# Kernel optimization log

Measured on AMD Instinct MI355X. Metric: run time of the kernel, lower is better.

## Reference

```python
import jax, jax.numpy as jnp
import numpy as np
import math

NUM_HEAD = 8
QK_DIM = 32       # in_dim // num_head
V_DIM = 32
KV_STRIDE = 2
Q_STRIDE = 1
LOCAL_RANGE = 16  # hard_range
POS_DIM = 256     # position_embedding_dim (= in_dim)
POS_MAG = 1.0
WAVE = 1000.0


def _position_feats(h, w, h_kv, w_kv, fcx_w, fcy_w):
    # sinusoidal embedding of (query_pos - key_pos), then linear projection per head
    fr = jnp.arange(POS_DIM // 4, dtype=jnp.float32)
    dim_mat = WAVE ** (4.0 / POS_DIM * fr)                 # (POS_DIM/4,)

    def emb(n_q, n_kv):
        diff = (jnp.arange(n_q, dtype=jnp.float32)[:, None] * Q_STRIDE
                - jnp.arange(n_kv, dtype=jnp.float32)[None, :] * KV_STRIDE) * POS_MAG
        a = diff[:, :, None] / dim_mat                      # (n_q, n_kv, POS_DIM/4)
        return jnp.concatenate([jnp.sin(a), jnp.cos(a)], axis=2)  # (n_q, n_kv, POS_DIM/2)

    inv_sqrt2 = 1.0 / math.sqrt(2.0)
    pfx = jnp.einsum('wkf,of->wko', emb(w, w_kv), fcx_w)
    pfx = pfx.reshape(w, w_kv, NUM_HEAD, QK_DIM).transpose(2, 0, 1, 3) * inv_sqrt2  # (H,w,w_kv,d)
    pfy = jnp.einsum('ykf,of->yko', emb(h, h_kv), fcy_w)
    pfy = pfy.reshape(h, h_kv, NUM_HEAD, QK_DIM).transpose(2, 0, 1, 3) * inv_sqrt2  # (H,h,h_kv,d)
    return pfx, pfy


def _local_mask(h, w, h_kv, w_kv):
    # True where attention is FORBIDDEN (matches masked_fill_ semantics of the map)
    R, s = LOCAL_RANGE, KV_STRIDE

    def axis_keep(n_q, n_kv):
        i = jnp.arange(n_q)
        k = jnp.arange(n_kv)
        lo = jnp.maximum((i - R) // s, 0)
        hi = (i + R + 1) // s + 1
        return (k[None, :] >= lo[:, None]) & (k[None, :] < hi[:, None])  # (n_q, n_kv)

    keep_y = axis_keep(h, h_kv)
    keep_x = axis_keep(w, w_kv)
    keep = keep_y[:, None, :, None] & keep_x[None, :, None, :]  # (h,w,h_kv,w_kv)
    return ~keep


def reference(x_input, q_w, k_w, v_w, fcx_w, fcy_w, appr_bias, geom_bias,
              proj_w, proj_b, gamma):
    n, c, h, w = x_input.shape
    H, d = NUM_HEAD, QK_DIM
    x_q = x_input                                   # q_stride == 1
    x_kv = x_input[:, :, ::KV_STRIDE, ::KV_STRIDE]  # AvgPool(kernel=1, stride=2)
    h_kv, w_kv = x_kv.shape[2], x_kv.shape[3]

    # 1x1 conv projections
    q = jnp.einsum('nchw,oc->nohw', x_q, q_w).reshape(n, H, d, h, w).transpose(0, 1, 3, 4, 2)  # (n,H,h,w,d)
    k = jnp.einsum('nchw,oc->nohw', x_kv, k_w).reshape(n, H, d, h_kv * w_kv)                   # (n,H,d,K)
    v = jnp.einsum('nchw,oc->nohw', x_kv, v_w).reshape(n, H, V_DIM, h_kv * w_kv).transpose(0, 1, 3, 2)  # (n,H,K,v)

    pfx, pfy = _position_feats(h, w, h_kv, w_kv, fcx_w, fcy_w)
    ab = appr_bias.reshape(1, H, 1, 1, d)
    gb = geom_bias.reshape(1, H, 1, 1, d)

    # appr-appr + bias-appr:  (q + appr_bias) @ k
    energy = jnp.einsum('nhyxd,nhdk->nhyxk', q + ab, k).reshape(n, H, h, w, h_kv, w_kv)
    # appr-position + bias-position, separable over x and y
    qg = q + gb
    energy = energy + jnp.einsum('nhyxd,hxkd->nhyxk', qg, pfx)[:, :, :, :, None, :]
    energy = energy + jnp.einsum('nhyxd,hykd->nhyxk', qg, pfy)[:, :, :, :, :, None]

    mask = _local_mask(h, w, h_kv, w_kv)  # (h,w,h_kv,w_kv), True = masked
    energy = jnp.where(mask[None, None], -jnp.inf, energy)
    energy = energy.reshape(n, H, h * w, h_kv * w_kv)

    attn = jax.nn.softmax(energy, axis=3)
    out = jnp.einsum('nhqk,nhkv->nhqv', attn, v)               # (n,H,h*w,v)
    out = out.transpose(0, 1, 3, 2).reshape(n, H * V_DIM, h, w)
    out = jnp.einsum('nchw,oc->nohw', out, proj_w) + proj_b[None, :, None, None]
    return gamma.reshape(()) * out + x_input


def setup_inputs() -> dict:
    key = jax.random.key(0)
    ks = jax.random.split(key, 11)
    s = 0.05  # keep attention logits in a sane range
    return {
        'x_input': jax.random.normal(ks[0], (2, 256, 64, 64), jnp.float32),
        'q_w': jax.random.normal(ks[1], (256, 256), jnp.float32) * s,
        'k_w': jax.random.normal(ks[2], (256, 256), jnp.float32) * s,
        'v_w': jax.random.normal(ks[3], (256, 256), jnp.float32) * s,
        'fcx_w': jax.random.normal(ks[4], (256, 128), jnp.float32) * s,
        'fcy_w': jax.random.normal(ks[5], (256, 128), jnp.float32) * s,
        'appr_bias': jax.random.normal(ks[6], (256,), jnp.float32) * s,
        'geom_bias': jax.random.normal(ks[7], (256,), jnp.float32) * s,
        'proj_w': jax.random.normal(ks[8], (256, 256), jnp.float32) * s,
        'proj_b': jax.random.normal(ks[9], (256,), jnp.float32) * s,
        'gamma': jax.random.normal(ks[10], (1,), jnp.float32),
    }
```

## Files before the change

### kernel.cpp

```cpp
#include <hip/hip_runtime.h>
#include <hip/hip_bf16.h>
#include <math.h>

#define NB   2
#define CC   256
#define PQ   4096
#define PKV  1024

#define M0 24.0f
#define EXSTRIDE 36
#define EYSTRIDE 20

typedef __attribute__((ext_vector_type(8))) short short8;
typedef __attribute__((ext_vector_type(4))) float f32x4;

__global__ __launch_bounds__(256) void prep_kernel(
    const float* __restrict__ q_w, const float* __restrict__ k_w,
    const float* __restrict__ v_w, const float* __restrict__ proj_w,
    __hip_bfloat16* __restrict__ qw_b, __hip_bfloat16* __restrict__ kw_b,
    __hip_bfloat16* __restrict__ vw_b, __hip_bfloat16* __restrict__ pw_b,
    const float* __restrict__ fcx, const float* __restrict__ fcy,
    __hip_bfloat16* __restrict__ pembx_b, __hip_bfloat16* __restrict__ pemby_b,
    const float* __restrict__ x, __hip_bfloat16* __restrict__ xb) {
  __shared__ __align__(16) float shbuf[64 * 65];
  const int bid = blockIdx.x;
  const int tid = threadIdx.x;
  if (bid < 256) {
    const int which = bid >> 6;
    const float* src = (which == 0) ? q_w : (which == 1) ? k_w
                       : (which == 2) ? v_w : proj_w;
    __hip_bfloat16* dst = (which == 0) ? qw_b : (which == 1) ? kw_b
                          : (which == 2) ? vw_b : pw_b;
    const int i = (bid & 63) * 256 + tid;
    const float4 v = reinterpret_cast<const float4*>(src)[i];
    short4 s;
    s.x = __builtin_bit_cast(short, __float2bfloat16(v.x));
    s.y = __builtin_bit_cast(short, __float2bfloat16(v.y));
    s.z = __builtin_bit_cast(short, __float2bfloat16(v.z));
    s.w = __builtin_bit_cast(short, __float2bfloat16(v.w));
    reinterpret_cast<short4*>(dst)[i] = s;
  } else if (bid < 508) {
    float* feat = shbuf;
    const int pb = bid - 256;
    const int dd = pb >> 1;
    const int which = pb & 1;
    const float* FC = which ? fcy : fcx;
    __hip_bfloat16* OUT = which ? pemby_b : pembx_b;
    if (tid < 64) {
      const float diff = (float)(dd - 62);
      const float dm = powf(1000.f, (float)tid * (1.f / 64.f));
      const float aa = diff / dm;
      feat[tid] = sinf(aa);
      feat[tid + 64] = cosf(aa);
    }
    __syncthreads();
    const float4* row4 = reinterpret_cast<const float4*>(FC + tid * 128);
    const float4* f4 = reinterpret_cast<const float4*>(feat);
    float s0 = 0.f, s1 = 0.f, s2 = 0.f, s3 = 0.f;
#pragma unroll
    for (int f = 0; f < 32; ++f) {
      const float4 fv = f4[f];
      const float4 rv = row4[f];
      s0 = fmaf(fv.x, rv.x, s0);
      s1 = fmaf(fv.y, rv.y, s1);
      s2 = fmaf(fv.z, rv.z, s2);
      s3 = fmaf(fv.w, rv.w, s3);
    }
    const float s = ((s0 + s1) + (s2 + s3)) * 0.70710678118654752440f;
    OUT[(size_t)dd * 256 + tid] = __float2bfloat16(s);
  } else {
    float (*t)[65] = reinterpret_cast<float(*)[65]>(shbuf);
    const int b = bid - 508;
    const int p0 = (b & 63) * 64;
    const int c0 = ((b >> 6) & 3) * 64;
    const int n = b >> 8;
    {
      const int pl = tid & 63, cg = tid >> 6;
#pragma unroll
      for (int i = 0; i < 16; ++i) {
        const int cl = cg * 16 + i;
        t[cl][pl] = x[((size_t)n * 256 + c0 + cl) * PQ + p0 + pl];
      }
    }
    __syncthreads();
    const int cl = tid & 63;
#pragma unroll
    for (int j = 0; j < 16; ++j) {
      const int pl = (tid >> 6) + 4 * j;
      ((__hip_bfloat16*)xb)[((size_t)n * PQ + p0 + pl) * 256 + c0 + cl] =
          __float2bfloat16(t[cl][pl]);
    }
  }
}

__global__ __launch_bounds__(256) void gemm_qkv_kernel(
    const __hip_bfloat16* __restrict__ xb,
    const __hip_bfloat16* __restrict__ qw, const __hip_bfloat16* __restrict__ kw,
    const __hip_bfloat16* __restrict__ vw, const float* __restrict__ ab,
    const float* __restrict__ gb, __hip_bfloat16* __restrict__ qab,
    __hip_bfloat16* __restrict__ qgb, __hip_bfloat16* __restrict__ k_lb,
    __hip_bfloat16* __restrict__ v_t) {
  __shared__ short bt[32 * 256];
  const int bid = blockIdx.x;
  const int tid = threadIdx.x;
  const int wv = tid >> 6, l = tid & 63, lc = l & 15, lq = l >> 4;

  const bool isQ = (bid < 1024);
  int n, o0, p0;
  bool isV = false;
  const __hip_bfloat16* W;
  if (isQ) {
    n = bid & 1;
    o0 = ((bid >> 1) & 3) * 64;
    p0 = (bid >> 3) * 32;
    W = qw;
  } else {
    const int kb2 = bid - 1024;
    n = kb2 & 1;
    o0 = ((kb2 >> 1) & 3) * 64;
    isV = ((kb2 >> 3) & 1) != 0;
    p0 = (kb2 >> 4) * 32;
    W = isV ? vw : kw;
  }

  {
    const int row = tid >> 3;
    const int pk = p0 + row;
    const int gp = isQ ? pk : ((pk >> 5) * 128 + (pk & 31) * 2);
    const short* src = (const short*)xb + ((size_t)n * PQ + gp) * 256;
#pragma unroll
    for (int j = 0; j < 4; ++j) {
      const int chunk = (tid & 7) + 8 * j;
      const int4 v = *reinterpret_cast<const int4*>(src + chunk * 8);
      *reinterpret_cast<int4*>(bt + row * 256 + ((chunk ^ (row & 7)) << 3)) = v;
    }
  }
  __syncthreads();

  const short* ar =
      (const short*)W + ((size_t)(o0 + wv * 16 + lc)) * 256 + 8 * lq;
  f32x4 acc0 = {0.f, 0.f, 0.f, 0.f};
  f32x4 acc1 = {0.f, 0.f, 0.f, 0.f};
#pragma unroll
  for (int kt = 0; kt < 8; ++kt) {
    const short8 af = *reinterpret_cast<const short8*>(ar + kt * 32);
    const int c0i = lq + 4 * kt;
    const short8 bf0 = *reinterpret_cast<const short8*>(
        bt + lc * 256 + ((c0i ^ (lc & 7)) << 3));
    const short8 bf1 = *reinterpret_cast<const short8*>(
        bt + (16 + lc) * 256 + ((c0i ^ ((16 + lc) & 7)) << 3));
    acc0 = __builtin_amdgcn_mfma_f32_16x16x32_bf16(af, bf0, acc0, 0, 0, 0);
    acc1 = __builtin_amdgcn_mfma_f32_16x16x32_bf16(af, bf1, acc1, 0, 0, 0);
  }

  if (isQ) {
#pragma unroll
    for (int r = 0; r < 4; ++r) {
      const int o = o0 + wv * 16 + 4 * lq + r;
      const float abo = ab[o], gbo = gb[o];
      const int head = o >> 5, dd = o & 31;
      const size_t gbase = (size_t)(n * 8 + head) * PQ;
      const float a_[2] = {acc0[r], acc1[r]};
#pragma unroll
      for (int nf = 0; nf < 2; ++nf) {
        const int p = p0 + 16 * nf + lc;
        const size_t idx = (gbase + p) * 32 + dd;
        qab[idx] = __float2bfloat16(a_[nf] + abo);
        qgb[idx] = __float2bfloat16(a_[nf] + gbo);
      }
    }
  } else {
#pragma unroll
    for (int r = 0; r < 4; ++r) {
      const int o = o0 + wv * 16 + 4 * lq + r;
      const int head = o >> 5, dd = o & 31;
      const float a_[2] = {acc0[r], acc1[r]};
#pragma unroll
      for (int nf = 0; nf < 2; ++nf) {
        const int p = p0 + 16 * nf + lc;
        if (!isV) {
          k_lb[((size_t)(n * 8 + head) * PKV + p) * 32 + dd] =
              __float2bfloat16(a_[nf]);
        } else {
          v_t[((size_t)(n * 8 + head) * 32 + dd) * PKV + p] =
              __float2bfloat16(a_[nf]);
        }
      }
    }
  }
}

__global__ __launch_bounds__(256) void ex_kernel(
    const __hip_bfloat16* __restrict__ qgb_b,
    const __hip_bfloat16* __restrict__ pembx_b,
    __hip_bfloat16* __restrict__ EX) {
  const int i = blockIdx.x;
  const int g = blockIdx.y;
  const int head = g & 7;
  const int wv = threadIdx.x >> 6;
  const int l = threadIdx.x & 63;
  const int lc = l & 15, lq = l >> 4;

  const int rowi = wv * 16 + lc;
  const int p = rowi * 64 + i;
  const short8 a = *reinterpret_cast<const short8*>(
      (const short*)qgb_b + ((size_t)g * PQ + p) * 32 + 8 * lq);

  const int drow0 = i - 2 * lc + 62;
  const int drow1 = i - 2 * (lc + 16) + 62;
  const short8 b0 = *reinterpret_cast<const short8*>(
      (const short*)pembx_b + (size_t)drow0 * 256 + head * 32 + 8 * lq);
  const short8 b1 = *reinterpret_cast<const short8*>(
      (const short*)pembx_b + (size_t)drow1 * 256 + head * 32 + 8 * lq);

  const f32x4 zero = {0.f, 0.f, 0.f, 0.f};
  const f32x4 c0 = __builtin_amdgcn_mfma_f32_16x16x32_bf16(a, b0, zero, 0, 0, 0);
  const f32x4 c1 = __builtin_amdgcn_mfma_f32_16x16x32_bf16(a, b1, zero, 0, 0, 0);

  const int lox = max((i - 16) >> 1, 0);
  const int hix = min(((i + 17) >> 1) + 1, 32);
#pragma unroll
  for (int r = 0; r < 4; ++r) {
    const int rowr = wv * 16 + 4 * lq + r;
    const int pr = rowr * 64 + i;
    __hip_bfloat16* o = EX + ((size_t)g * PQ + pr) * EXSTRIDE;
    o[lc] = __float2bfloat16(
        (lc >= lox && lc < hix) ? (c0[r] - M0) : -1e30f);
    o[16 + lc] = __float2bfloat16(
        (lc + 16 >= lox && lc + 16 < hix) ? (c1[r] - M0) : -1e30f);
    if (lc < 4) o[32 + lc] = __float2bfloat16(-1e30f);
  }
}

__global__ __launch_bounds__(512, 8) void attn_mfma_kernel(
    const __hip_bfloat16* __restrict__ qab_b,
    const __hip_bfloat16* __restrict__ qgb_b,
    const __hip_bfloat16* __restrict__ k_lb,
    const __hip_bfloat16* __restrict__ v_t,
    const __hip_bfloat16* __restrict__ EX,
    const __hip_bfloat16* __restrict__ pemby_b,
    __hip_bfloat16* __restrict__ attb) {
  const int g = blockIdx.y;
  const int nImg = g >> 3, hd = g & 7;
  const int bx = blockIdx.x & 3;
  const int by = blockIdx.x >> 2;
  const int tx = bx * 16;
  const int wv = threadIdx.x >> 6;
  const int yw = wv & 3;
  const int s = wv >> 2;
  const int y = by * 4 + yw;
  const int l = threadIdx.x & 63;
  const int lc = l & 15;
  const int lq = l >> 4;

  __shared__ float eybuf[4][EYSTRIDE][16];
  __shared__ float mrg[4][64][9];
  __shared__ float obuf[4][16][33];

  const int KLO = max((tx - 16) >> 1, 0);
  const int lo_y = max((y - 16) >> 1, 0);
  const int hi_y = min(((y + 17) >> 1) + 1, 32);
  const int NKY = hi_y - lo_y;

  const int xq = tx + lc;
  const int pq_ = y * 64 + xq;

  const short8 qa = *reinterpret_cast<const short8*>(
      (const short*)qab_b + ((size_t)g * PQ + pq_) * 32 + 8 * lq);

  const short* exr = (const short*)EX + ((size_t)g * PQ + pq_) * EXSTRIDE;
  float exC0[4], exC1[4];
#pragma unroll
  for (int r = 0; r < 4; ++r) {
    exC0[r] = __bfloat162float(
        __builtin_bit_cast(__hip_bfloat16, exr[KLO + 4 * lq + r]));
    exC1[r] = __bfloat162float(
        __builtin_bit_cast(__hip_bfloat16, exr[min(KLO + 16 + 4 * lq + r, 35)]));
  }

  if (s == 0) {
    const short8 ag = *reinterpret_cast<const short8*>(
        (const short*)qgb_b + ((size_t)g * PQ + pq_) * 32 + 8 * lq);
    const int dr0 = y - 2 * (lo_y + lc) + 62;
    const int dr1 = y - 2 * (lo_y + lc + 16) + 62;
    const short8 pb0 = *reinterpret_cast<const short8*>(
        (const short*)pemby_b + (size_t)dr0 * 256 + hd * 32 + 8 * lq);
    const short8 pb1 = *reinterpret_cast<const short8*>(
        (const short*)pemby_b + (size_t)dr1 * 256 + hd * 32 + 8 * lq);
    const f32x4 zero = {0.f, 0.f, 0.f, 0.f};
    const f32x4 e0 = __builtin_amdgcn_mfma_f32_16x16x32_bf16(ag, pb0, zero, 0, 0, 0);
    const f32x4 e1 = __builtin_amdgcn_mfma_f32_16x16x32_bf16(ag, pb1, zero, 0, 0, 0);
#pragma unroll
    for (int r = 0; r < 4; ++r) eybuf[yw][lc][4 * lq + r] = e0[r];
    if (lc < 4) {
#pragma unroll
      for (int r = 0; r < 4; ++r) eybuf[yw][16 + lc][4 * lq + r] = e1[r];
    }
  }
  __syncthreads();

  const __hip_bfloat16* kb =
      k_lb + ((size_t)g * PKV + (size_t)lo_y * 32) * 32;
  const __hip_bfloat16* kb0 = kb + (KLO + lc) * 32 + 8 * lq;
  const __hip_bfloat16* kb1 = kb + min(KLO + 16 + lc, 31) * 32 + 8 * lq;
  const __hip_bfloat16* vb0 =
      v_t + ((size_t)g * 32 + lc) * PKV + (size_t)lo_y * 32 + KLO + 8 * lq;
  const __hip_bfloat16* vb1 = vb0 + 16 * PKV;

  f32x4 acc0 = {0.f, 0.f, 0.f, 0.f};
  f32x4 acc1 = {0.f, 0.f, 0.f, 0.f};
  float lp = 0.f;
  const int srcA = lc + ((l & 16) << 1);
  const int srcB = srcA + 16;
  const bool hiL = (l & 32) != 0;

#pragma unroll 1
  for (int t = s; t < NKY; t += 2) {
    const short8 k0 = *reinterpret_cast<const short8*>(kb0 + t * 1024);
    const short8 k1 = *reinterpret_cast<const short8*>(kb1 + t * 1024);
    const short8 v0 = *reinterpret_cast<const short8*>(vb0 + t * 32);
    const short8 v1 = *reinterpret_cast<const short8*>(vb1 + t * 32);
    const f32x4 zero = {0.f, 0.f, 0.f, 0.f};
    const f32x4 s0 = __builtin_amdgcn_mfma_f32_16x16x32_bf16(k0, qa, zero, 0, 0, 0);
    const f32x4 s1 = __builtin_amdgcn_mfma_f32_16x16x32_bf16(k1, qa, zero, 0, 0, 0);
    const float eyC = eybuf[yw][t][lc];
    float p0[4], p1[4];
#pragma unroll
    for (int r = 0; r < 4; ++r) {
      p0[r] = __expf(s0[r] + exC0[r] + eyC);
      p1[r] = __expf(s1[r] + exC1[r] + eyC);
    }
    lp += ((p0[0] + p0[1]) + (p0[2] + p0[3])) +
          ((p1[0] + p1[1]) + (p1[2] + p1[3]));
    int w00, w01, w10, w11;
    asm("v_cvt_pk_bf16_f32 %0, %1, %2" : "=v"(w00) : "v"(p0[0]), "v"(p0[1]));
    asm("v_cvt_pk_bf16_f32 %0, %1, %2" : "=v"(w01) : "v"(p0[2]), "v"(p0[3]));
    asm("v_cvt_pk_bf16_f32 %0, %1, %2" : "=v"(w10) : "v"(p1[0]), "v"(p1[1]));
    asm("v_cvt_pk_bf16_f32 %0, %1, %2" : "=v"(w11) : "v"(p1[2]), "v"(p1[3]));
    const int a0 = __shfl(w00, srcA, 64), b0 = __shfl(w10, srcA, 64);
    const int a1 = __shfl(w01, srcA, 64), b1 = __shfl(w11, srcA, 64);
    const int a2 = __shfl(w00, srcB, 64), b2 = __shfl(w10, srcB, 64);
    const int a3 = __shfl(w01, srcB, 64), b3 = __shfl(w11, srcB, 64);
    int4 pw;
    pw.x = hiL ? b0 : a0;
    pw.y = hiL ? b1 : a1;
    pw.z = hiL ? b2 : a2;
    pw.w = hiL ? b3 : a3;
    const short8 pf = __builtin_bit_cast(short8, pw);
    acc0 = __builtin_amdgcn_mfma_f32_16x16x32_bf16(pf, v0, acc0, 0, 0, 0);
    acc1 = __builtin_amdgcn_mfma_f32_16x16x32_bf16(pf, v1, acc1, 0, 0, 0);
  }

  if (s == 1) {
    float* m = mrg[yw][l];
#pragma unroll
    for (int r = 0; r < 4; ++r) m[r] = acc0[r];
#pragma unroll
    for (int r = 0; r < 4; ++r) m[4 + r] = acc1[r];
    m[8] = lp;
  }
  __syncthreads();
  if (s == 1) return;
  {
    const float* m = mrg[yw][l];
#pragma unroll
    for (int r = 0; r < 4; ++r) acc0[r] += m[r];
#pragma unroll
    for (int r = 0; r < 4; ++r) acc1[r] += m[4 + r];
    lp += m[8];
  }

  lp += __shfl_xor(lp, 16);
  lp += __shfl_xor(lp, 32);
  const float invall = 1.f / lp;

#pragma unroll
  for (int r = 0; r < 4; ++r) {
    const float inv = __shfl(invall, 4 * lq + r, 16);
    obuf[yw][4 * lq + r][lc] = acc0[r] * inv;
    obuf[yw][4 * lq + r][16 + lc] = acc1[r] * inv;
  }
  const int qp = l >> 2;
  const int ch = (l & 3) * 8;
  short8 sv;
#pragma unroll
  for (int j = 0; j < 8; ++j)
    sv[j] = __builtin_bit_cast(short, __float2bfloat16(obuf[yw][qp][ch + j]));
  const int p = y * 64 + tx + qp;
  *reinterpret_cast<short8*>(
      (short*)attb + ((size_t)nImg * PQ + p) * 256 + hd * 32 + ch) = sv;
}

__global__ __launch_bounds__(256) void gemm_out_kernel(
    const __hip_bfloat16* __restrict__ attb,
    const __hip_bfloat16* __restrict__ pw, const float* __restrict__ pb,
    const float* __restrict__ gamma, const float* __restrict__ x_in,
    float* __restrict__ out) {
  __shared__ short bt[32 * 256];
  const int p0 = blockIdx.x * 32;
  const int o0 = blockIdx.y * 64;
  const int n = blockIdx.z;
  const int tid = threadIdx.x;
  const int wv = tid >> 6, l = tid & 63, lc = l & 15, lq = l >> 4;

  {
    const int row = tid >> 3;
    const short* src = (const short*)attb + ((size_t)n * PQ + p0 + row) * 256;
#pragma unroll
    for (int j = 0; j < 4; ++j) {
      const int chunk = (tid & 7) + 8 * j;
      const int4 v = *reinterpret_cast<const int4*>(src + chunk * 8);
      *reinterpret_cast<int4*>(bt + row * 256 + ((chunk ^ (row & 7)) << 3)) = v;
    }
  }
  __syncthreads();

  const short* ar =
      (const short*)pw + ((size_t)(o0 + wv * 16 + lc)) * 256 + 8 * lq;
  f32x4 acc0 = {0.f, 0.f, 0.f, 0.f};
  f32x4 acc1 = {0.f, 0.f, 0.f, 0.f};
#pragma unroll
  for (int kt = 0; kt < 8; ++kt) {
    const short8 af = *reinterpret_cast<const short8*>(ar + kt * 32);
    const int c0i = lq + 4 * kt;
    const short8 bf0 = *reinterpret_cast<const short8*>(
        bt + lc * 256 + ((c0i ^ (lc & 7)) << 3));
    const short8 bf1 = *reinterpret_cast<const short8*>(
        bt + (16 + lc) * 256 + ((c0i ^ ((16 + lc) & 7)) << 3));
    acc0 = __builtin_amdgcn_mfma_f32_16x16x32_bf16(af, bf0, acc0, 0, 0, 0);
    acc1 = __builtin_amdgcn_mfma_f32_16x16x32_bf16(af, bf1, acc1, 0, 0, 0);
  }
  const float gm = gamma[0];
#pragma unroll
  for (int r = 0; r < 4; ++r) {
    const int o = o0 + wv * 16 + 4 * lq + r;
    const float bo = pb[o];
    const size_t obase = ((size_t)n * 256 + o) * PQ;
    const size_t i0 = obase + (p0 + 0 + lc);
    const size_t i1 = obase + (p0 + 16 + lc);
    out[i0] = fmaf(gm, acc0[r] + bo, x_in[i0]);
    out[i1] = fmaf(gm, acc1[r] + bo, x_in[i1]);
  }
}

extern "C" void kernel_launch(void* const* d_in, const int* in_sizes, int n_in,
                              void* d_out, int out_size, void* d_ws,
                              size_t ws_size, hipStream_t stream) {
  const float* x = (const float*)d_in[0];
  const float* q_w = (const float*)d_in[1];
  const float* k_w = (const float*)d_in[2];
  const float* v_w = (const float*)d_in[3];
  const float* fcx_w = (const float*)d_in[4];
  const float* fcy_w = (const float*)d_in[5];
  const float* ab = (const float*)d_in[6];
  const float* gb = (const float*)d_in[7];
  const float* proj_w = (const float*)d_in[8];
  const float* proj_b = (const float*)d_in[9];
  const float* gamma = (const float*)d_in[10];
  float* out = (float*)d_out;

  __hip_bfloat16* bp = (__hip_bfloat16*)d_ws;
  __hip_bfloat16* EX = bp;      bp += 2359296;
  __hip_bfloat16* qab_b = bp;   bp += 2097152;
  __hip_bfloat16* qgb_b = bp;   bp += 2097152;
  __hip_bfloat16* k_lb = bp;    bp += 524288;
  __hip_bfloat16* v_t = bp;     bp += 524288;
  __hip_bfloat16* pembx_b = bp; bp += 32256;
  __hip_bfloat16* pemby_b = bp; bp += 32256;
  __hip_bfloat16* qw_b = bp;    bp += 65536;
  __hip_bfloat16* kw_b = bp;    bp += 65536;
  __hip_bfloat16* vw_b = bp;    bp += 65536;
  __hip_bfloat16* pw_b = bp;    bp += 65536;
  __hip_bfloat16* xb = bp;      bp += 2097152;
  __hip_bfloat16* attb = bp;    bp += 2097152;

  prep_kernel<<<dim3(1020), 256, 0, stream>>>(q_w, k_w, v_w, proj_w, qw_b,
                                              kw_b, vw_b, pw_b, fcx_w, fcy_w,
                                              pembx_b, pemby_b, x, xb);
  gemm_qkv_kernel<<<dim3(1536), 256, 0, stream>>>(xb, qw_b, kw_b, vw_b, ab,
                                                  gb, qab_b, qgb_b, k_lb, v_t);
  ex_kernel<<<dim3(64, 16), 256, 0, stream>>>(qgb_b, pembx_b, EX);
  attn_mfma_kernel<<<dim3(64, 16), 512, 0, stream>>>(qab_b, qgb_b, k_lb, v_t,
                                                     EX, pemby_b, attb);
  gemm_out_kernel<<<dim3(128, 4, 2), 256, 0, stream>>>(attb, pw_b, proj_b,
                                                       gamma, x, out);
}
```

Baseline: 75.89 us.

## Drop split-K across wave pairs in attention; give each wave its own query row

Each 512-thread block previously covered 4 query rows, with two waves per row splitting the key-row loop and merging partial accumulators through shared memory. Now each of the 8 waves owns one query row and runs the full key loop, which removes the merge buffer, the extra barrier and the early exit of half the waves. The grid is halved to keep full coverage. This cuts merge overhead but makes each wave's serial loop twice as long, leaving less parallelism to hide latency.

```diff
diff --git a/kernel.cpp b/kernel.cpp
--- a/kernel.cpp
+++ b/kernel.cpp
@@ -242,20 +242,17 @@
     __hip_bfloat16* __restrict__ attb) {
   const int g = blockIdx.y;
   const int nImg = g >> 3, hd = g & 7;
-  const int bx = blockIdx.x & 3;
-  const int by = blockIdx.x >> 2;
-  const int tx = bx * 16;
-  const int wv = threadIdx.x >> 6;
-  const int yw = wv & 3;
-  const int s = wv >> 2;
-  const int y = by * 4 + yw;
+  const int tile = blockIdx.x;
+  const int tx = (tile & 3) * 16;
+  const int ty = (tile >> 2) * 8;
+  const int w = threadIdx.x >> 6;
+  const int y = ty + w;
   const int l = threadIdx.x & 63;
   const int lc = l & 15;
   const int lq = l >> 4;
 
-  __shared__ float eybuf[4][EYSTRIDE][16];
-  __shared__ float mrg[4][64][9];
-  __shared__ float obuf[4][16][33];
+  __shared__ float eybuf[8][EYSTRIDE][16];
+  __shared__ float obuf[8][16][33];
 
   const int KLO = max((tx - 16) >> 1, 0);
   const int lo_y = max((y - 16) >> 1, 0);
@@ -278,7 +275,7 @@
         __builtin_bit_cast(__hip_bfloat16, exr[min(KLO + 16 + 4 * lq + r, 35)]));
   }
 
-  if (s == 0) {
+  {
     const short8 ag = *reinterpret_cast<const short8*>(
         (const short*)qgb_b + ((size_t)g * PQ + pq_) * 32 + 8 * lq);
     const int dr0 = y - 2 * (lo_y + lc) + 62;
@@ -291,10 +288,10 @@
     const f32x4 e0 = __builtin_amdgcn_mfma_f32_16x16x32_bf16(ag, pb0, zero, 0, 0, 0);
     const f32x4 e1 = __builtin_amdgcn_mfma_f32_16x16x32_bf16(ag, pb1, zero, 0, 0, 0);
 #pragma unroll
-    for (int r = 0; r < 4; ++r) eybuf[yw][lc][4 * lq + r] = e0[r];
+    for (int r = 0; r < 4; ++r) eybuf[w][lc][4 * lq + r] = e0[r];
     if (lc < 4) {
 #pragma unroll
-      for (int r = 0; r < 4; ++r) eybuf[yw][16 + lc][4 * lq + r] = e1[r];
+      for (int r = 0; r < 4; ++r) eybuf[w][16 + lc][4 * lq + r] = e1[r];
     }
   }
   __syncthreads();
@@ -315,7 +312,7 @@
   const bool hiL = (l & 32) != 0;
 
 #pragma unroll 1
-  for (int t = s; t < NKY; t += 2) {
+  for (int t = 0; t < NKY; ++t) {
     const short8 k0 = *reinterpret_cast<const short8*>(kb0 + t * 1024);
     const short8 k1 = *reinterpret_cast<const short8*>(kb1 + t * 1024);
     const short8 v0 = *reinterpret_cast<const short8*>(vb0 + t * 32);
@@ -323,7 +320,7 @@
     const f32x4 zero = {0.f, 0.f, 0.f, 0.f};
     const f32x4 s0 = __builtin_amdgcn_mfma_f32_16x16x32_bf16(k0, qa, zero, 0, 0, 0);
     const f32x4 s1 = __builtin_amdgcn_mfma_f32_16x16x32_bf16(k1, qa, zero, 0, 0, 0);
-    const float eyC = eybuf[yw][t][lc];
+    const float eyC = eybuf[w][t][lc];
     float p0[4], p1[4];
 #pragma unroll
     for (int r = 0; r < 4; ++r) {
@@ -351,25 +348,6 @@
     acc1 = __builtin_amdgcn_mfma_f32_16x16x32_bf16(pf, v1, acc1, 0, 0, 0);
   }
 
-  if (s == 1) {
-    float* m = mrg[yw][l];
-#pragma unroll
-    for (int r = 0; r < 4; ++r) m[r] = acc0[r];
-#pragma unroll
-    for (int r = 0; r < 4; ++r) m[4 + r] = acc1[r];
-    m[8] = lp;
-  }
-  __syncthreads();
-  if (s == 1) return;
-  {
-    const float* m = mrg[yw][l];
-#pragma unroll
-    for (int r = 0; r < 4; ++r) acc0[r] += m[r];
-#pragma unroll
-    for (int r = 0; r < 4; ++r) acc1[r] += m[4 + r];
-    lp += m[8];
-  }
-
   lp += __shfl_xor(lp, 16);
   lp += __shfl_xor(lp, 32);
   const float invall = 1.f / lp;
@@ -377,15 +355,15 @@
 #pragma unroll
   for (int r = 0; r < 4; ++r) {
     const float inv = __shfl(invall, 4 * lq + r, 16);
-    obuf[yw][4 * lq + r][lc] = acc0[r] * inv;
-    obuf[yw][4 * lq + r][16 + lc] = acc1[r] * inv;
+    obuf[w][4 * lq + r][lc] = acc0[r] * inv;
+    obuf[w][4 * lq + r][16 + lc] = acc1[r] * inv;
   }
   const int qp = l >> 2;
   const int ch = (l & 3) * 8;
   short8 sv;
 #pragma unroll
   for (int j = 0; j < 8; ++j)
-    sv[j] = __builtin_bit_cast(short, __float2bfloat16(obuf[yw][qp][ch + j]));
+    sv[j] = __builtin_bit_cast(short, __float2bfloat16(obuf[w][qp][ch + j]));
   const int p = y * 64 + tx + qp;
   *reinterpret_cast<short8*>(
       (short*)attb + ((size_t)nImg * PQ + p) * 256 + hd * 32 + ch) = sv;
@@ -480,7 +458,7 @@
   gemm_qkv_kernel<<<dim3(1536), 256, 0, stream>>>(xb, qw_b, kw_b, vw_b, ab,
                                                   gb, qab_b, qgb_b, k_lb, v_t);
   ex_kernel<<<dim3(64, 16), 256, 0, stream>>>(qgb_b, pembx_b, EX);
-  attn_mfma_kernel<<<dim3(64, 16), 512, 0, stream>>>(qab_b, qgb_b, k_lb, v_t,
+  attn_mfma_kernel<<<dim3(32, 16), 512, 0, stream>>>(qab_b, qgb_b, k_lb, v_t,
                                                      EX, pemby_b, attb);
   gemm_out_kernel<<<dim3(128, 4, 2), 256, 0, stream>>>(attb, pw_b, proj_b,
                                                        gamma, x, out);
```

After: 74.93 us. Within noise of the previous version (-1.3%).
